# Optimization experiments

Measured on AMD Instinct MI355X. Metric: run time of the kernel, lower is better.

## Reference

```python
import jax, jax.numpy as jnp
import numpy as np

B, H, M, DH = 8, 32, 8, 64  # batch, spatial h=w, heads, dim_head
C = M * DH
HW = H * H


def _make_pos_idx(h: int) -> np.ndarray:
    # A[i, j] = j - i, matching tf.constant([range(i, i+h) for i in range(0, -h, -1)])
    A = np.arange(h)[None, :] - np.arange(h)[:, None]
    horiz = np.tile(A, (h, h))                              # (h^2, h^2)
    vert = np.repeat(np.repeat(A, h, axis=0), h, axis=1)    # (h^2, h^2)
    return (2 * h - 1) * (vert + h - 1) + (horiz + h - 1)   # values in [0, (2h-1)^2)


def setup_inputs() -> dict:
    key = jax.random.key(0)
    ks = jax.random.split(key, 4)
    x = jax.random.normal(ks[0], (B, H, H, C), dtype=jnp.float32)
    w_qkv = jax.random.normal(ks[1], (DH, 3 * DH), dtype=jnp.float32) * (1.0 / np.sqrt(DH))
    b_qkv = jnp.zeros((3 * DH,), dtype=jnp.float32)
    w_ht = jax.random.normal(ks[2], (C, C), dtype=jnp.float32) * (1.0 / np.sqrt(C))
    b_ht = jnp.zeros((C,), dtype=jnp.float32)
    # Glorot-normal scalar table over (2h-1)^2 relative positions
    n_rel = (2 * H - 1) ** 2
    pos_table = jax.random.normal(ks[3], (n_rel,), dtype=jnp.float32) * np.float32(np.sqrt(2.0 / (n_rel + 1)))
    pos_idx = jnp.asarray(_make_pos_idx(H), dtype=jnp.int32)  # (HW, HW)
    return {"x": x, "w_qkv": w_qkv, "b_qkv": b_qkv, "w_ht": w_ht, "b_ht": b_ht,
            "pos_table": pos_table, "pos_idx": pos_idx}


def reference(x, w_qkv, b_qkv, w_ht, b_ht, pos_table, pos_idx):
    b, h, w, c = x.shape
    d_h = c // M
    # split heads into the batch dim: (b*M, h, w, d_h)
    xh = x.reshape(b, h, w, M, d_h).transpose(0, 3, 1, 2, 4).reshape(b * M, h, w, d_h)
    # 1x1 conv == per-pixel dense
    qkv = xh @ w_qkv + b_qkv                       # (b*M, h, w, 3*DH)
    qkv = qkv.reshape(b * M, h * w, DH, 3)
    q, k, v = qkv[..., 0], qkv[..., 1], qkv[..., 2]
    q = q / jnp.sqrt(jnp.float32(DH))
    att = jnp.einsum('bic,bjc->bij', q, k)         # (b*M, HW, HW)
    pos_emb = pos_table[pos_idx]                   # (HW, HW) gathered bias
    att = jax.nn.softmax(att + pos_emb, axis=-1)
    o = jnp.einsum('bij,bjc->bic', att, v)         # (b*M, HW, DH)
    o = o.reshape(b, M, h, w, d_h).transpose(0, 2, 3, 1, 4).reshape(b, h, w, c)
    out = o @ w_ht + b_ht                          # 1x1 head_transform conv
    return (out, att, pos_emb)
```

## Files before the change

kernel.cpp:

```cpp
#include <hip/hip_runtime.h>
#include <hip/hip_bf16.h>

typedef __attribute__((ext_vector_type(8))) __bf16 bf16x8;
typedef __attribute__((ext_vector_type(8))) short  s16x8;
typedef __attribute__((ext_vector_type(4))) float  f32x4;

#define HW2 1024
#define CDIM 512

static __device__ __forceinline__ unsigned short f2b(float f) {
  __hip_bfloat16 h = __float2bfloat16(f);
  return __builtin_bit_cast(unsigned short, h);
}

static __device__ __forceinline__ f32x4 mfma16(s16x8 a, s16x8 b, f32x4 c) {
  return __builtin_amdgcn_mfma_f32_16x16x32_bf16(
      __builtin_bit_cast(bf16x8, a), __builtin_bit_cast(bf16x8, b), c, 0, 0, 0);
}


__global__ __launch_bounds__(256) void k_prep_wqkv(const float* __restrict__ w,
    unsigned short* __restrict__ Wtq, unsigned short* __restrict__ Wtk,
    unsigned short* __restrict__ Wtv) {
  int i = blockIdx.x * 256 + threadIdx.x;
  int c = i >> 6, k = i & 63;
  const float* src = w + k * 192 + 3 * c;
  Wtq[i] = f2b(src[0] * 0.125f);
  Wtk[i] = f2b(src[1]);
  Wtv[i] = f2b(src[2]);
}

__global__ __launch_bounds__(256) void k_prep_wht(const float* __restrict__ w,
                                                  unsigned short* __restrict__ WhtT) {
  int i = blockIdx.x * 256 + threadIdx.x;
  int c = i >> 9, k = i & 511;
  WhtT[i] = f2b(w[k * 512 + c]);
}

__global__ __launch_bounds__(256) void k_posemb(const float* __restrict__ table,
    const int* __restrict__ idx, float* __restrict__ pe) {
  int i = blockIdx.x * 256 + threadIdx.x;
  #pragma unroll
  for (int j = 0; j < 4; ++j) {
    int p = i + j * 262144;
    pe[p] = table[idx[p]];
  }
}

__global__ __launch_bounds__(256) void k_qkv(const float* __restrict__ x,
    const float* __restrict__ b_qkv,
    const unsigned short* __restrict__ Wtq, const unsigned short* __restrict__ Wtk,
    const unsigned short* __restrict__ Wtv,
    unsigned short* __restrict__ Qb, unsigned short* __restrict__ Kb,
    unsigned short* __restrict__ Vb) {
  int bm = blockIdx.x >> 4;
  int pt = blockIdx.x & 15;
  int wid = threadIdx.x >> 6, lane = threadIdx.x & 63;
  int l15 = lane & 15, lg = lane >> 4;
  int b = bm >> 3, m = bm & 7;
  int pbase = pt * 64 + wid * 16;

  int pA = pbase + l15;
  const float* xp = x + (size_t)(b * HW2 + pA) * CDIM + m * 64 + lg * 8;
  f32x4 xv0 = *(const f32x4*)(xp);
  f32x4 xv1 = *(const f32x4*)(xp + 4);
  f32x4 xv2 = *(const f32x4*)(xp + 32);
  f32x4 xv3 = *(const f32x4*)(xp + 36);
  s16x8 a0, a1;
  #pragma unroll
  for (int j = 0; j < 4; ++j) {
    a0[j]     = (short)f2b(xv0[j]);
    a0[4 + j] = (short)f2b(xv1[j]);
    a1[j]     = (short)f2b(xv2[j]);
    a1[4 + j] = (short)f2b(xv3[j]);
  }

  f32x4 acc[12];
  #pragma unroll
  for (int ct = 0; ct < 12; ++ct) acc[ct] = (f32x4){0.f, 0.f, 0.f, 0.f};

  #pragma unroll
  for (int ct = 0; ct < 12; ++ct) {
    const unsigned short* W = (ct < 4) ? Wtq : (ct < 8 ? Wtk : Wtv);
    int c = (ct & 3) * 16 + l15;
    const unsigned short* wp = W + c * 64 + lg * 8;
    s16x8 b0 = *(const s16x8*)(wp);
    s16x8 b1 = *(const s16x8*)(wp + 32);
    acc[ct] = mfma16(a0, b0, acc[ct]);
    acc[ct] = mfma16(a1, b1, acc[ct]);
  }

  #pragma unroll
  for (int ct = 0; ct < 12; ++ct) {
    int s = ct >> 2;
    int c = (ct & 3) * 16 + l15;
    float bias = b_qkv[3 * c + s];
    if (s == 0) bias *= 0.125f;
    unsigned short* D = (s == 0) ? Qb : (s == 1 ? Kb : Vb);
    #pragma unroll
    for (int i = 0; i < 4; ++i) {
      int p = pbase + lg * 4 + i;
      D[(size_t)(bm * HW2 + p) * 64 + c] = f2b(acc[ct][i] + bias);
    }
  }
}

__global__ __launch_bounds__(256) void k_transpose_v(const unsigned short* __restrict__ Vb,
                                                     unsigned short* __restrict__ Vt) {
  int bm = blockIdx.x >> 4;
  int pt = blockIdx.x & 15;
  __shared__ unsigned short tile[64][80];
  int t = threadIdx.x;
  int p = t & 63, dq = t >> 6;
  const unsigned short* src = Vb + (size_t)(bm * HW2 + pt * 64 + p) * 64 + dq * 16;
  s16x8 v0 = *(const s16x8*)src;
  s16x8 v1 = *(const s16x8*)(src + 8);
  *(s16x8*)&tile[p][dq * 16] = v0;
  *(s16x8*)&tile[p][dq * 16 + 8] = v1;
  __syncthreads();
  int dh = t & 63, pq = t >> 6;
  s16x8 o0, o1;
  #pragma unroll
  for (int j = 0; j < 8; ++j) {
    o0[j] = (short)tile[pq * 16 + j][dh];
    o1[j] = (short)tile[pq * 16 + 8 + j][dh];
  }
  unsigned short* dst = Vt + (size_t)(bm * 64 + dh) * HW2 + pt * 64 + pq * 16;
  *(s16x8*)dst = o0;
  *(s16x8*)(dst + 8) = o1;
}

__global__ __launch_bounds__(256, 4) void k_attn(
    const unsigned short* __restrict__ Qb, const unsigned short* __restrict__ Kb,
    const unsigned short* __restrict__ Vt, const float* __restrict__ pos_emb,
    float* __restrict__ att, unsigned short* __restrict__ O) {
  int bm = blockIdx.x >> 6;
  int qt = blockIdx.x & 63;
  int wid = threadIdx.x >> 6, lane = threadIdx.x & 63;
  int l15 = lane & 15, lg = lane >> 4;

  __shared__ unsigned short P[16][1032];
  __shared__ float redm[4][16];
  __shared__ float reds[4][16];

  const unsigned short* qp = Qb + (size_t)(bm * HW2 + qt * 16 + l15) * 64 + lg * 8;
  s16x8 qa0 = *(const s16x8*)qp;
  s16x8 qa1 = *(const s16x8*)(qp + 32);

  f32x4 acc[16];
  const unsigned short* kbase = Kb + (size_t)bm * HW2 * 64;
  #pragma unroll
  for (int ct = 0; ct < 16; ++ct) {
    int col = wid * 256 + ct * 16 + l15;
    const unsigned short* kp = kbase + (size_t)col * 64 + lg * 8;
    s16x8 kb0 = *(const s16x8*)kp;
    s16x8 kb1 = *(const s16x8*)(kp + 32);
    f32x4 a = (f32x4){0.f, 0.f, 0.f, 0.f};
    a = mfma16(qa0, kb0, a);
    a = mfma16(qa1, kb1, a);
    acc[ct] = a;
  }

  float pmax[4] = {-1e30f, -1e30f, -1e30f, -1e30f};
  #pragma unroll
  for (int ct = 0; ct < 16; ++ct) {
    int col = wid * 256 + ct * 16 + l15;
    #pragma unroll
    for (int i = 0; i < 4; ++i) {
      int qr = qt * 16 + lg * 4 + i;
      float v = acc[ct][i] + pos_emb[(size_t)qr * HW2 + col];
      acc[ct][i] = v;
      pmax[i] = fmaxf(pmax[i], v);
    }
  }
  #pragma unroll
  for (int i = 0; i < 4; ++i) {
    #pragma unroll
    for (int mk = 1; mk < 16; mk <<= 1)
      pmax[i] = fmaxf(pmax[i], __shfl_xor(pmax[i], mk));
  }
  if (l15 == 0) {
    #pragma unroll
    for (int i = 0; i < 4; ++i) redm[wid][lg * 4 + i] = pmax[i];
  }
  __syncthreads();
  float mrow[4];
  #pragma unroll
  for (int i = 0; i < 4; ++i) {
    int r = lg * 4 + i;
    mrow[i] = fmaxf(fmaxf(redm[0][r], redm[1][r]), fmaxf(redm[2][r], redm[3][r]));
  }

  float psum[4] = {0.f, 0.f, 0.f, 0.f};
  #pragma unroll
  for (int ct = 0; ct < 16; ++ct) {
    #pragma unroll
    for (int i = 0; i < 4; ++i) {
      float e = __expf(acc[ct][i] - mrow[i]);
      acc[ct][i] = e;
      psum[i] += e;
    }
  }
  #pragma unroll
  for (int i = 0; i < 4; ++i) {
    #pragma unroll
    for (int mk = 1; mk < 16; mk <<= 1) psum[i] += __shfl_xor(psum[i], mk);
  }
  if (l15 == 0) {
    #pragma unroll
    for (int i = 0; i < 4; ++i) reds[wid][lg * 4 + i] = psum[i];
  }
  __syncthreads();
  float inv[4];
  #pragma unroll
  for (int i = 0; i < 4; ++i) {
    int r = lg * 4 + i;
    inv[i] = 1.0f / (reds[0][r] + reds[1][r] + reds[2][r] + reds[3][r]);
  }

  float* abase = att + (size_t)(bm * HW2 + qt * 16) * HW2;
  #pragma unroll
  for (int ct = 0; ct < 16; ++ct) {
    int col = wid * 256 + ct * 16 + l15;
    #pragma unroll
    for (int i = 0; i < 4; ++i) {
      int rl = lg * 4 + i;
      float v = acc[ct][i] * inv[i];
      abase[(size_t)rl * HW2 + col] = v;
      P[rl][col] = f2b(v);
    }
  }
  __syncthreads();

  f32x4 o = (f32x4){0.f, 0.f, 0.f, 0.f};
  const unsigned short* vbase = Vt + (size_t)(bm * 64 + wid * 16 + l15) * HW2;
  #pragma unroll
  for (int kt = 0; kt < 32; ++kt) {
    s16x8 pa = *(const s16x8*)&P[l15][kt * 32 + lg * 8];
    s16x8 vb = *(const s16x8*)(vbase + kt * 32 + lg * 8);
    o = mfma16(pa, vb, o);
  }
  unsigned short* obase = O + (size_t)(bm * HW2 + qt * 16) * 64 + wid * 16 + l15;
  #pragma unroll
  for (int i = 0; i < 4; ++i) obase[(size_t)(lg * 4 + i) * 64] = f2b(o[i]);
}

__global__ __launch_bounds__(256) void k_ht(
    const unsigned short* __restrict__ O, const unsigned short* __restrict__ WhtT,
    const float* __restrict__ b_ht, float* __restrict__ out) {
  int rt = blockIdx.x >> 1;
  int ch = blockIdx.x & 1;
  int wid = threadIdx.x >> 6, lane = threadIdx.x & 63;
  int wr = wid >> 1, wc = wid & 1;
  int l15 = lane & 15, lg = lane >> 4;
  int b = (rt * 32) >> 10;
  int p0 = (rt * 32) & 1023;

  __shared__ unsigned short A[32][520];

  int t = threadIdx.x;
  #pragma unroll
  for (int j = 0; j < 8; ++j) {
    int idx = t * 8 + j * 2048;
    int row = idx >> 9;
    int k0 = idx & 511;
    int m = k0 >> 6, kk = k0 & 63;
    const unsigned short* src = O + (size_t)((b * 8 + m) * HW2 + p0 + row) * 64 + kk;
    *(s16x8*)&A[row][k0] = *(const s16x8*)src;
  }
  __syncthreads();

  f32x4 acc[8];
  #pragma unroll
  for (int ct = 0; ct < 8; ++ct) acc[ct] = (f32x4){0.f, 0.f, 0.f, 0.f};

  #pragma unroll
  for (int kt = 0; kt < 16; ++kt) {
    s16x8 a = *(const s16x8*)&A[wr * 16 + l15][kt * 32 + lg * 8];
    #pragma unroll
    for (int ct = 0; ct < 8; ++ct) {
      int col = ch * 256 + wc * 128 + ct * 16 + l15;
      s16x8 bf = *(const s16x8*)(WhtT + (size_t)col * 512 + kt * 32 + lg * 8);
      acc[ct] = mfma16(a, bf, acc[ct]);
    }
  }

  #pragma unroll
  for (int ct = 0; ct < 8; ++ct) {
    int col = ch * 256 + wc * 128 + ct * 16 + l15;
    float bias = b_ht[col];
    #pragma unroll
    for (int i = 0; i < 4; ++i) {
      int rp = rt * 32 + wr * 16 + lg * 4 + i;
      out[(size_t)rp * 512 + col] = acc[ct][i] + bias;
    }
  }
}

extern "C" void kernel_launch(void* const* d_in, const int* in_sizes, int n_in,
                              void* d_out, int out_size, void* d_ws, size_t ws_size,
                              hipStream_t stream) {
  const float* x         = (const float*)d_in[0];
  const float* w_qkv     = (const float*)d_in[1];
  const float* b_qkv     = (const float*)d_in[2];
  const float* w_ht      = (const float*)d_in[3];
  const float* b_ht      = (const float*)d_in[4];
  const float* pos_table = (const float*)d_in[5];
  const int*   pos_idx   = (const int*)d_in[6];

  float* out = (float*)d_out;
  float* att = out + 4194304;
  float* pe  = att + 67108864;

  char* ws = (char*)d_ws;
  unsigned short* Qb   = (unsigned short*)(ws);
  unsigned short* Kb   = (unsigned short*)(ws + (8u  << 20));
  unsigned short* Vb   = (unsigned short*)(ws + (16u << 20));
  unsigned short* Vt   = (unsigned short*)(ws + (24u << 20));
  unsigned short* O    = (unsigned short*)(ws + (32u << 20));
  unsigned short* Wtq  = (unsigned short*)(ws + (40u << 20));
  unsigned short* Wtk  = Wtq + 4096;
  unsigned short* Wtv  = Wtk + 4096;
  unsigned short* WhtT = (unsigned short*)(ws + (40u << 20) + 65536);

  k_prep_wqkv<<<16,   256, 0, stream>>>(w_qkv, Wtq, Wtk, Wtv);
  k_prep_wht <<<1024, 256, 0, stream>>>(w_ht, WhtT);
  k_posemb   <<<1024, 256, 0, stream>>>(pos_table, pos_idx, pe);
  k_qkv      <<<1024, 256, 0, stream>>>(x, b_qkv, Wtq, Wtk, Wtv, Qb, Kb, Vb);
  k_transpose_v<<<1024, 256, 0, stream>>>(Vb, Vt);
  k_attn     <<<4096, 256, 0, stream>>>(Qb, Kb, Vt, pe, att, O);
  k_ht       <<<512,  256, 0, stream>>>(O, WhtT, b_ht, out);
}
```

Before: 226.4 us.

## Fuse prep kernels, fold V transpose into QKV, index pos table directly

Merges the three weight/pos-embedding prep kernels into one launch. Stages Q, K and transposed V in shared memory inside the QKV kernel so rows are stored coalesced, which removes the separate V transpose kernel and its workspace round trip. In attention, the bias is read from the small pos table using a closed-form index instead of the full 1024x1024 gathered matrix, cutting heavy global reads. The output tile is also staged in shared memory for vector stores. The closed-form index assumes pos_idx always follows the fixed relative-position formula.

Result: faster. 211.3 us (-6.7%).

```diff
diff --git a/kernel.cpp b/kernel.cpp
--- a/kernel.cpp
+++ b/kernel.cpp
@@ -3,6 +3,7 @@
 
 typedef __attribute__((ext_vector_type(8))) __bf16 bf16x8;
 typedef __attribute__((ext_vector_type(8))) short  s16x8;
+typedef __attribute__((ext_vector_type(4))) short  s16x4;
 typedef __attribute__((ext_vector_type(4))) float  f32x4;
 
 #define HW2 1024
@@ -18,32 +19,31 @@
       __builtin_bit_cast(bf16x8, a), __builtin_bit_cast(bf16x8, b), c, 0, 0, 0);
 }
 
-
-__global__ __launch_bounds__(256) void k_prep_wqkv(const float* __restrict__ w,
+__global__ __launch_bounds__(256) void k_prep(
+    const float* __restrict__ w_qkv, const float* __restrict__ w_ht,
+    const float* __restrict__ table, const int* __restrict__ idx,
     unsigned short* __restrict__ Wtq, unsigned short* __restrict__ Wtk,
-    unsigned short* __restrict__ Wtv) {
-  int i = blockIdx.x * 256 + threadIdx.x;
-  int c = i >> 6, k = i & 63;
-  const float* src = w + k * 192 + 3 * c;
-  Wtq[i] = f2b(src[0] * 0.125f);
-  Wtk[i] = f2b(src[1]);
-  Wtv[i] = f2b(src[2]);
-}
-
-__global__ __launch_bounds__(256) void k_prep_wht(const float* __restrict__ w,
-                                                  unsigned short* __restrict__ WhtT) {
-  int i = blockIdx.x * 256 + threadIdx.x;
-  int c = i >> 9, k = i & 511;
-  WhtT[i] = f2b(w[k * 512 + c]);
-}
-
-__global__ __launch_bounds__(256) void k_posemb(const float* __restrict__ table,
-    const int* __restrict__ idx, float* __restrict__ pe) {
-  int i = blockIdx.x * 256 + threadIdx.x;
-  #pragma unroll
-  for (int j = 0; j < 4; ++j) {
-    int p = i + j * 262144;
-    pe[p] = table[idx[p]];
+    unsigned short* __restrict__ Wtv, unsigned short* __restrict__ WhtT,
+    float* __restrict__ pe) {
+  int blk = blockIdx.x;
+  if (blk < 16) {
+    int i = blk * 256 + threadIdx.x;
+    int c = i >> 6, k = i & 63;
+    const float* src = w_qkv + k * 192 + 3 * c;
+    Wtq[i] = f2b(src[0] * 0.125f);
+    Wtk[i] = f2b(src[1]);
+    Wtv[i] = f2b(src[2]);
+  } else if (blk < 1040) {
+    int i = (blk - 16) * 256 + threadIdx.x;
+    int c = i >> 9, k = i & 511;
+    WhtT[i] = f2b(w_ht[k * 512 + c]);
+  } else {
+    int i = (blk - 1040) * 256 + threadIdx.x;
+    #pragma unroll
+    for (int j = 0; j < 4; ++j) {
+      int p = i + j * 262144;
+      pe[p] = table[idx[p]];
+    }
   }
 }
 
@@ -52,13 +52,15 @@
     const unsigned short* __restrict__ Wtq, const unsigned short* __restrict__ Wtk,
     const unsigned short* __restrict__ Wtv,
     unsigned short* __restrict__ Qb, unsigned short* __restrict__ Kb,
-    unsigned short* __restrict__ Vb) {
+    unsigned short* __restrict__ Vt) {
   int bm = blockIdx.x >> 4;
   int pt = blockIdx.x & 15;
   int wid = threadIdx.x >> 6, lane = threadIdx.x & 63;
   int l15 = lane & 15, lg = lane >> 4;
   int b = bm >> 3, m = bm & 7;
   int pbase = pt * 64 + wid * 16;
+
+  __shared__ unsigned short T[64][200];
 
   int pA = pbase + l15;
   const float* xp = x + (size_t)(b * HW2 + pA) * CDIM + m * 64 + lg * 8;
@@ -90,49 +92,38 @@
     acc[ct] = mfma16(a1, b1, acc[ct]);
   }
 
+  int lrow = wid * 16 + lg * 4;
   #pragma unroll
   for (int ct = 0; ct < 12; ++ct) {
     int s = ct >> 2;
     int c = (ct & 3) * 16 + l15;
     float bias = b_qkv[3 * c + s];
     if (s == 0) bias *= 0.125f;
-    unsigned short* D = (s == 0) ? Qb : (s == 1 ? Kb : Vb);
-    #pragma unroll
-    for (int i = 0; i < 4; ++i) {
-      int p = pbase + lg * 4 + i;
-      D[(size_t)(bm * HW2 + p) * 64 + c] = f2b(acc[ct][i] + bias);
-    }
-  }
-}
-
-__global__ __launch_bounds__(256) void k_transpose_v(const unsigned short* __restrict__ Vb,
-                                                     unsigned short* __restrict__ Vt) {
-  int bm = blockIdx.x >> 4;
-  int pt = blockIdx.x & 15;
-  __shared__ unsigned short tile[64][80];
+    #pragma unroll
+    for (int i = 0; i < 4; ++i) {
+      unsigned short hv = f2b(acc[ct][i] + bias);
+      if (s == 0)      T[lrow + i][c] = hv;
+      else if (s == 1) T[lrow + i][64 + c] = hv;
+      else             T[c][128 + lrow + i] = hv;
+    }
+  }
+  __syncthreads();
+
   int t = threadIdx.x;
-  int p = t & 63, dq = t >> 6;
-  const unsigned short* src = Vb + (size_t)(bm * HW2 + pt * 64 + p) * 64 + dq * 16;
-  s16x8 v0 = *(const s16x8*)src;
-  s16x8 v1 = *(const s16x8*)(src + 8);
-  *(s16x8*)&tile[p][dq * 16] = v0;
-  *(s16x8*)&tile[p][dq * 16 + 8] = v1;
-  __syncthreads();
-  int dh = t & 63, pq = t >> 6;
-  s16x8 o0, o1;
-  #pragma unroll
-  for (int j = 0; j < 8; ++j) {
-    o0[j] = (short)tile[pq * 16 + j][dh];
-    o1[j] = (short)tile[pq * 16 + 8 + j][dh];
-  }
-  unsigned short* dst = Vt + (size_t)(bm * 64 + dh) * HW2 + pt * 64 + pq * 16;
-  *(s16x8*)dst = o0;
-  *(s16x8*)(dst + 8) = o1;
+  int r = t >> 2, cp = t & 3;
+  size_t prow = (size_t)(bm * HW2 + pt * 64 + r) * 64 + cp * 16;
+  *(s16x8*)(Qb + prow)     = *(const s16x8*)&T[r][cp * 16];
+  *(s16x8*)(Qb + prow + 8) = *(const s16x8*)&T[r][cp * 16 + 8];
+  *(s16x8*)(Kb + prow)     = *(const s16x8*)&T[r][64 + cp * 16];
+  *(s16x8*)(Kb + prow + 8) = *(const s16x8*)&T[r][64 + cp * 16 + 8];
+  size_t vrow = ((size_t)bm * 64 + r) * HW2 + pt * 64 + cp * 16;
+  *(s16x8*)(Vt + vrow)     = *(const s16x8*)&T[r][128 + cp * 16];
+  *(s16x8*)(Vt + vrow + 8) = *(const s16x8*)&T[r][128 + cp * 16 + 8];
 }
 
 __global__ __launch_bounds__(256, 4) void k_attn(
     const unsigned short* __restrict__ Qb, const unsigned short* __restrict__ Kb,
-    const unsigned short* __restrict__ Vt, const float* __restrict__ pos_emb,
+    const unsigned short* __restrict__ Vt, const float* __restrict__ ptab,
     float* __restrict__ att, unsigned short* __restrict__ O) {
   int bm = blockIdx.x >> 6;
   int qt = blockIdx.x & 63;
@@ -142,6 +133,7 @@
   __shared__ unsigned short P[16][1032];
   __shared__ float redm[4][16];
   __shared__ float reds[4][16];
+  __shared__ unsigned short Osm[16][68];
 
   const unsigned short* qp = Qb + (size_t)(bm * HW2 + qt * 16 + l15) * 64 + lg * 8;
   s16x8 qa0 = *(const s16x8*)qp;
@@ -161,14 +153,15 @@
     acc[ct] = a;
   }
 
+  int cbase = 1984 - 63 * (qt >> 1) - ((qt & 1) << 4) - lg * 4;
   float pmax[4] = {-1e30f, -1e30f, -1e30f, -1e30f};
   #pragma unroll
   for (int ct = 0; ct < 16; ++ct) {
     int col = wid * 256 + ct * 16 + l15;
-    #pragma unroll
-    for (int i = 0; i < 4; ++i) {
-      int qr = qt * 16 + lg * 4 + i;
-      float v = acc[ct][i] + pos_emb[(size_t)qr * HW2 + col];
+    int t0 = 63 * (col >> 5) + (col & 31) + cbase;
+    #pragma unroll
+    for (int i = 0; i < 4; ++i) {
+      float v = acc[ct][i] + ptab[t0 - i];
       acc[ct][i] = v;
       pmax[i] = fmaxf(pmax[i], v);
     }
@@ -240,9 +233,14 @@
     s16x8 vb = *(const s16x8*)(vbase + kt * 32 + lg * 8);
     o = mfma16(pa, vb, o);
   }
-  unsigned short* obase = O + (size_t)(bm * HW2 + qt * 16) * 64 + wid * 16 + l15;
-  #pragma unroll
-  for (int i = 0; i < 4; ++i) obase[(size_t)(lg * 4 + i) * 64] = f2b(o[i]);
+
+  #pragma unroll
+  for (int i = 0; i < 4; ++i) Osm[lg * 4 + i][wid * 16 + l15] = f2b(o[i]);
+  __syncthreads();
+  int t = threadIdx.x;
+  int row = t >> 4, cpo = t & 15;
+  unsigned short* dst = O + (size_t)(bm * HW2 + qt * 16 + row) * 64 + cpo * 4;
+  *(s16x4*)dst = *(const s16x4*)&Osm[row][cpo * 4];
 }
 
 __global__ __launch_bounds__(256) void k_ht(
@@ -315,19 +313,16 @@
   char* ws = (char*)d_ws;
   unsigned short* Qb   = (unsigned short*)(ws);
   unsigned short* Kb   = (unsigned short*)(ws + (8u  << 20));
-  unsigned short* Vb   = (unsigned short*)(ws + (16u << 20));
-  unsigned short* Vt   = (unsigned short*)(ws + (24u << 20));
-  unsigned short* O    = (unsigned short*)(ws + (32u << 20));
-  unsigned short* Wtq  = (unsigned short*)(ws + (40u << 20));
+  unsigned short* Vt   = (unsigned short*)(ws + (16u << 20));
+  unsigned short* O    = (unsigned short*)(ws + (24u << 20));
+  unsigned short* Wtq  = (unsigned short*)(ws + (32u << 20));
   unsigned short* Wtk  = Wtq + 4096;
   unsigned short* Wtv  = Wtk + 4096;
-  unsigned short* WhtT = (unsigned short*)(ws + (40u << 20) + 65536);
-
-  k_prep_wqkv<<<16,   256, 0, stream>>>(w_qkv, Wtq, Wtk, Wtv);
-  k_prep_wht <<<1024, 256, 0, stream>>>(w_ht, WhtT);
-  k_posemb   <<<1024, 256, 0, stream>>>(pos_table, pos_idx, pe);
-  k_qkv      <<<1024, 256, 0, stream>>>(x, b_qkv, Wtq, Wtk, Wtv, Qb, Kb, Vb);
-  k_transpose_v<<<1024, 256, 0, stream>>>(Vb, Vt);
-  k_attn     <<<4096, 256, 0, stream>>>(Qb, Kb, Vt, pe, att, O);
-  k_ht       <<<512,  256, 0, stream>>>(O, WhtT, b_ht, out);
-}
+  unsigned short* WhtT = (unsigned short*)(ws + (32u << 20) + 65536);
+
+  k_prep<<<2064, 256, 0, stream>>>(w_qkv, w_ht, pos_table, pos_idx,
+                                   Wtq, Wtk, Wtv, WhtT, pe);
+  k_qkv <<<1024, 256, 0, stream>>>(x, b_qkv, Wtq, Wtk, Wtv, Qb, Kb, Vt);
+  k_attn<<<4096, 256, 0, stream>>>(Qb, Kb, Vt, pos_table, att, O);
+  k_ht  <<<512,  256, 0, stream>>>(O, WhtT, b_ht, out);
+}
```
